# Performance work log

Hardware: AMD Instinct MI355X
Metric: run time of the kernel (lower is better)

Reference implementation:

```python
import jax, jax.numpy as jnp
import numpy as np

K = 20          # neighbors
EPS = 1e-5      # batch-norm eps (torch default)


def setup_inputs() -> dict:
    key = jax.random.key(0)
    k1, k2 = jax.random.split(key, 2)
    B, C, N = 16, 3, 2048
    out_dims, in_dims = 64, 2 * C
    x = jax.random.normal(k1, (B, C, N), dtype=jnp.float32)
    # Conv2d 1x1 weight, kaiming-style init as in init_layer: std = sqrt(2/(1*1*out))
    W = jax.random.normal(k2, (out_dims, in_dims), dtype=jnp.float32) * np.float32(np.sqrt(2.0 / out_dims))
    bn_weight = jnp.ones((out_dims,), dtype=jnp.float32)
    bn_bias = jnp.zeros((out_dims,), dtype=jnp.float32)
    return {"x": x, "W": W, "bn_weight": bn_weight, "bn_bias": bn_bias}


def _get_graph_feature(x, k):
    # x: (B, C, N)
    xx = jnp.sum(x * x, axis=1)                       # (B, N) squared norms
    inner = jnp.einsum('bcn,bcm->bnm', x, x)          # (B, N, N)
    pd = -xx[:, :, None] + 2.0 * inner - xx[:, None, :]  # -||xi - xj||^2
    _, idx = jax.lax.top_k(pd, k)                     # (B, N, k) nearest neighbors
    xt = jnp.transpose(x, (0, 2, 1))                  # (B, N, C)
    # gather neighbor features per batch: (N, C)[ (N, k) ] -> (N, k, C)
    neigh = jax.vmap(lambda feats, ind: feats[ind])(xt, idx)   # (B, N, k, C)
    center = jnp.broadcast_to(xt[:, :, None, :], neigh.shape)  # (B, N, k, C)
    feat = jnp.concatenate([neigh - center, center], axis=-1)  # (B, N, k, 2C)
    return jnp.transpose(feat, (0, 3, 1, 2))          # (B, 2C, N, k)


def reference(x, W, bn_weight, bn_bias):
    feat = _get_graph_feature(x, K)                   # (B, 2C, N, k)
    y = jnp.einsum('oc,bcnk->bonk', W, feat)          # 1x1 conv, no bias
    # BatchNorm2d_fw: fresh running stats + training=True -> plain batch stats
    mean = jnp.mean(y, axis=(0, 2, 3), keepdims=True)
    var = jnp.var(y, axis=(0, 2, 3), keepdims=True)   # biased variance
    yn = (y - mean) * jax.lax.rsqrt(var + EPS)
    yn = yn * bn_weight[None, :, None, None] + bn_bias[None, :, None, None]
    out = jnp.max(jax.nn.relu(yn), axis=-1)           # max over k -> (B, 64, N)
    return out
```

## Files before the change

### kernel.cpp

```cpp
#include <hip/hip_runtime.h>
#include <math.h>

#define B_   16
#define N_   2048
#define KNN  20
#define OD   64
#define M_TOT (B_ * N_ * KNN)
#define PPB  64
#define NB   64
#define CAP  89
#define BKT_BASE 468

typedef unsigned long long u64;
typedef unsigned int u32;

__global__ __launch_bounds__(256, 2) void k1_knn(const float* __restrict__ x,
                                                 float* __restrict__ stats,
                                                 int* __restrict__ idxbuf) {
    __shared__ float4 pts[N_];
    __shared__ u64    coll[PPB][CAP];
    __shared__ u32    pcnt[PPB];
    __shared__ u32    edgev[PPB];

    u32* hist = (u32*)&coll[0][0];

    const int b     = blockIdx.x >> 5;
    const int chunk = blockIdx.x & 31;
    const int t     = threadIdx.x;

    const float* xb = x + b * 3 * N_;
    for (int n = t; n < N_; n += 256) {
        float x0 = xb[n], x1 = xb[N_ + n], x2 = xb[2 * N_ + n];
        float xx = x0 * x0;
        xx = fmaf(x1, x1, xx);
        xx = fmaf(x2, x2, xx);
        pts[n] = make_float4(x0, x1, x2, xx);
    }
    {
        uint4* h4 = (uint4*)hist;
        for (int i = t; i < NB * PPB / 4; i += 256) h4[i] = make_uint4(0, 0, 0, 0);
        if (t < PPB) pcnt[t] = 0;
    }
    __syncthreads();

    const int p  = t & 63;
    const int s  = t >> 6;
    const int il = chunk * 64 + p;
    const float4 pi = pts[il];
    const int j0 = s << 9;

    {
        auto binit = [&](const float4& pj) {
            float dot = pi.x * pj.x;
            dot = fmaf(pi.y, pj.y, dot);
            dot = fmaf(pi.z, pj.z, dot);
            float pd = fmaf(2.f, dot, -pi.w) - pj.w;
            u32 nk = __float_as_uint(pd) & 0x7FFFFFFFu;
            int bkt = (int)(nk >> 21) - BKT_BASE;
            bkt = min(max(bkt, 0), 63);
            atomicAdd(&hist[bkt * PPB + p], 1u);
        };
        for (int jj = 0; jj < 512; jj += 4) {
            int j = j0 + jj;
            float4 q0 = pts[j + 0];
            float4 q1 = pts[j + 1];
            float4 q2 = pts[j + 2];
            float4 q3 = pts[j + 3];
            binit(q0); binit(q1); binit(q2); binit(q3);
        }
    }
    __syncthreads();

    if (t < PPB) {
        int cum = 0, tau = 63;
        for (int k = 0; k < NB; ++k) {
            cum += (int)hist[k * PPB + t];
            if (cum >= KNN) { tau = k; break; }
        }
        edgev[t] = (u32)(BKT_BASE + 1 + tau) << 21;
    }
    __syncthreads();

    {
        const u32 edge = edgev[p];
        auto collect = [&](const float4& pj, int j) {
            float dot = pi.x * pj.x;
            dot = fmaf(pi.y, pj.y, dot);
            dot = fmaf(pi.z, pj.z, dot);
            float pd = fmaf(2.f, dot, -pi.w) - pj.w;
            u32 u = __float_as_uint(pd);
            u32 nk = u & 0x7FFFFFFFu;
            if (nk < edge) {
                u32 mono = ((int)u < 0) ? ~u : (u | 0x80000000u);
                u64 key = ((u64)mono << 32) | (u32)(~j);
                u32 pos = atomicAdd(&pcnt[p], 1u);
                if (pos < CAP) coll[p][pos] = key;
            }
        };
        for (int jj = 0; jj < 512; jj += 4) {
            int j = j0 + jj;
            float4 q0 = pts[j + 0];
            float4 q1 = pts[j + 1];
            float4 q2 = pts[j + 2];
            float4 q3 = pts[j + 3];
            collect(q0, j + 0); collect(q1, j + 1);
            collect(q2, j + 2); collect(q3, j + 3);
        }
    }
    __syncthreads();

    if (t < PPB) {
        const int cnt = min((int)pcnt[t], CAP);
        u64 d[KNN];
#pragma unroll
        for (int q = 0; q < KNN; ++q) d[q] = 0ull;
        for (int e = 0; e < cnt; ++e) {
            u64 v = coll[t][e];
#pragma unroll
            for (int q = 0; q < KNN; ++q) {
                u64 hi = (v > d[q]) ? v : d[q];
                u64 lo = (v > d[q]) ? d[q] : v;
                d[q] = hi; v = lo;
            }
        }
        int ri[KNN];
#pragma unroll
        for (int r = 0; r < KNN; ++r) ri[r] = ~(u32)d[r];

        int* op = idxbuf + (b * N_ + il) * KNN;
#pragma unroll
        for (int r = 0; r < KNN; ++r) op[r] = ri[r];

        float se0 = 0.f, se1 = 0.f, se2 = 0.f;
        float see[6] = {0.f, 0.f, 0.f, 0.f, 0.f, 0.f};
#pragma unroll
        for (int r = 0; r < KNN; ++r) {
            float4 pj = pts[ri[r]];
            float e0 = pj.x - pi.x, e1 = pj.y - pi.y, e2 = pj.z - pi.z;
            se0 += e0; se1 += e1; se2 += e2;
            see[0] = fmaf(e0, e0, see[0]);
            see[1] = fmaf(e0, e1, see[1]);
            see[2] = fmaf(e0, e2, see[2]);
            see[3] = fmaf(e1, e1, see[3]);
            see[4] = fmaf(e1, e2, see[4]);
            see[5] = fmaf(e2, e2, see[5]);
        }
        float c0 = pi.x, c1 = pi.y, c2 = pi.z;
        float v[27];
        v[0] = se0; v[1] = se1; v[2] = se2;
        v[3] = 20.f * c0; v[4] = 20.f * c1; v[5] = 20.f * c2;
        v[6]  = see[0];
        v[7]  = see[1];
        v[8]  = see[2];
        v[9]  = se0 * c0;
        v[10] = se0 * c1;
        v[11] = se0 * c2;
        v[12] = see[3];
        v[13] = see[4];
        v[14] = se1 * c0;
        v[15] = se1 * c1;
        v[16] = se1 * c2;
        v[17] = see[5];
        v[18] = se2 * c0;
        v[19] = se2 * c1;
        v[20] = se2 * c2;
        v[21] = 20.f * c0 * c0;
        v[22] = 20.f * c0 * c1;
        v[23] = 20.f * c0 * c2;
        v[24] = 20.f * c1 * c1;
        v[25] = 20.f * c1 * c2;
        v[26] = 20.f * c2 * c2;

#pragma unroll
        for (int m = 0; m < 27; ++m) {
            float sm = v[m];
#pragma unroll
            for (int off = 32; off > 0; off >>= 1) sm += __shfl_xor(sm, off);
            if (t == 0) atomicAdd(stats + m, sm);
        }
    }
}

__global__ void k2_fin(const float* __restrict__ stats, const float* __restrict__ W,
                       const float* __restrict__ bnw, const float* __restrict__ bnb,
                       float* __restrict__ wp) {
    const int o = threadIdx.x;
    float m[6];
#pragma unroll
    for (int c = 0; c < 6; ++c) m[c] = stats[c];
    float S[6][6];
    int p = 6;
#pragma unroll
    for (int a = 0; a < 6; ++a)
#pragma unroll
        for (int bb = a; bb < 6; ++bb) { S[a][bb] = stats[p]; S[bb][a] = stats[p]; ++p; }
    float w[6];
#pragma unroll
    for (int c = 0; c < 6; ++c) w[c] = W[o * 6 + c];

    const float invM = 1.f / (float)M_TOT;
    float mean = 0.f;
#pragma unroll
    for (int c = 0; c < 6; ++c) mean += w[c] * m[c];
    mean *= invM;
    float ey2 = 0.f;
#pragma unroll
    for (int a = 0; a < 6; ++a)
#pragma unroll
        for (int bb = 0; bb < 6; ++bb) ey2 += w[a] * w[bb] * S[a][bb];
    ey2 *= invM;
    float var   = ey2 - mean * mean;
    float scale = bnw[o] * rsqrtf(var + 1e-5f);
    float shift = bnb[o] - mean * scale;
#pragma unroll
    for (int c = 0; c < 6; ++c) wp[o * 8 + c] = w[c] * scale;
    wp[o * 8 + 6] = shift;
    wp[o * 8 + 7] = 0.f;
}

__global__ __launch_bounds__(256) void k3_out(const float* __restrict__ x,
                                              const float* __restrict__ wp,
                                              const int* __restrict__ idxbuf,
                                              float* __restrict__ out) {
    __shared__ float4 pts[N_];
    __shared__ float  lwp[OD * 8];

    const int b     = blockIdx.x >> 4;
    const int chunk = blockIdx.x & 15;
    const int t     = threadIdx.x;

    const float* xb = x + b * 3 * N_;
    for (int n = t; n < N_; n += 256)
        pts[n] = make_float4(xb[n], xb[N_ + n], xb[2 * N_ + n], 0.f);
    for (int q = t; q < OD * 8; q += 256) lwp[q] = wp[q];
    __syncthreads();

    const int n = chunk * 128 + (t & 127);
    const int h = t >> 7;
    const float4 pi = pts[n];
    const int* ip = idxbuf + (b * N_ + n) * KNN;

    float e0[KNN], e1[KNN], e2[KNN];
#pragma unroll
    for (int r = 0; r < KNN; ++r) {
        int j = ip[r];
        float4 pj = pts[j];
        e0[r] = pj.x - pi.x;
        e1[r] = pj.y - pi.y;
        e2[r] = pj.z - pi.z;
    }

    float* ob = out + (size_t)b * OD * N_ + n;
    const int o0 = h * 32;
#pragma unroll 8
    for (int o = o0; o < o0 + 32; ++o) {
        float w0 = lwp[o * 8 + 0], w1 = lwp[o * 8 + 1], w2 = lwp[o * 8 + 2];
        float w3 = lwp[o * 8 + 3], w4 = lwp[o * 8 + 4], w5 = lwp[o * 8 + 5];
        float base = lwp[o * 8 + 6];
        base = fmaf(w3, pi.x, base);
        base = fmaf(w4, pi.y, base);
        base = fmaf(w5, pi.z, base);
        float acc = 0.f;
#pragma unroll
        for (int r = 0; r < KNN; ++r) {
            float y = base;
            y = fmaf(w0, e0[r], y);
            y = fmaf(w1, e1[r], y);
            y = fmaf(w2, e2[r], y);
            acc = fmaxf(acc, y);
        }
        ob[(size_t)o * N_] = acc;
    }
}

extern "C" void kernel_launch(void* const* d_in, const int* in_sizes, int n_in,
                              void* d_out, int out_size, void* d_ws, size_t ws_size,
                              hipStream_t stream) {
    const float* x   = (const float*)d_in[0];
    const float* W   = (const float*)d_in[1];
    const float* bnw = (const float*)d_in[2];
    const float* bnb = (const float*)d_in[3];
    float* out = (float*)d_out;

    float* stats  = (float*)d_ws;
    float* wp     = (float*)((char*)d_ws + 1024);
    int*   idxbuf = (int*)((char*)d_ws + 4096);

    hipMemsetAsync(d_ws, 0, 128, stream);
    k1_knn<<<dim3(512), dim3(256), 0, stream>>>(x, stats, idxbuf);
    k2_fin<<<dim3(1), dim3(64), 0, stream>>>(stats, W, bnw, bnb, wp);
    k3_out<<<dim3(256), dim3(256), 0, stream>>>(x, wp, idxbuf, out);
}
```

Before: 264.9 us.

## Widen kNN blocks, store 16-bit candidate indices, recompute distances in selection

k1 now runs 512 threads per block, so each point's candidate scan is split across 8 slices of 256 instead of 4 of 512. Candidates are stored as 16-bit indices instead of 64-bit keys, which shrinks shared memory and allows a separate histogram buffer. Distances are recomputed in the single-thread selection phase, and an early reject against the current 20th-best skips the insertion network. k3 uses 512 blocks of 64 points with indices staged in shared memory and 16 outputs per thread. The cost is recomputing distances in the selection phase, which is still serial, and k1 now carries a 4-blocks-per-SM launch bound on 512-thread blocks.

```diff
diff --git a/kernel.cpp b/kernel.cpp
--- a/kernel.cpp
+++ b/kernel.cpp
@@ -8,65 +8,58 @@
 #define M_TOT (B_ * N_ * KNN)
 #define PPB  64
 #define NB   64
-#define CAP  89
+#define CAP  96
 #define BKT_BASE 468
 
 typedef unsigned long long u64;
 typedef unsigned int u32;
-
-__global__ __launch_bounds__(256, 2) void k1_knn(const float* __restrict__ x,
+typedef unsigned short u16;
+
+__global__ __launch_bounds__(512, 4) void k1_knn(const float* __restrict__ x,
                                                  float* __restrict__ stats,
                                                  int* __restrict__ idxbuf) {
     __shared__ float4 pts[N_];
-    __shared__ u64    coll[PPB][CAP];
+    __shared__ u32    hist[NB * PPB];
+    __shared__ u16    coll[PPB][CAP];
     __shared__ u32    pcnt[PPB];
     __shared__ u32    edgev[PPB];
-
-    u32* hist = (u32*)&coll[0][0];
 
     const int b     = blockIdx.x >> 5;
     const int chunk = blockIdx.x & 31;
     const int t     = threadIdx.x;
 
     const float* xb = x + b * 3 * N_;
-    for (int n = t; n < N_; n += 256) {
+    for (int n = t; n < N_; n += 512) {
         float x0 = xb[n], x1 = xb[N_ + n], x2 = xb[2 * N_ + n];
         float xx = x0 * x0;
         xx = fmaf(x1, x1, xx);
         xx = fmaf(x2, x2, xx);
         pts[n] = make_float4(x0, x1, x2, xx);
     }
-    {
-        uint4* h4 = (uint4*)hist;
-        for (int i = t; i < NB * PPB / 4; i += 256) h4[i] = make_uint4(0, 0, 0, 0);
-        if (t < PPB) pcnt[t] = 0;
-    }
+    for (int i = t; i < NB * PPB; i += 512) hist[i] = 0;
+    if (t < PPB) pcnt[t] = 0;
     __syncthreads();
 
     const int p  = t & 63;
     const int s  = t >> 6;
     const int il = chunk * 64 + p;
     const float4 pi = pts[il];
-    const int j0 = s << 9;
-
-    {
-        auto binit = [&](const float4& pj) {
-            float dot = pi.x * pj.x;
-            dot = fmaf(pi.y, pj.y, dot);
-            dot = fmaf(pi.z, pj.z, dot);
-            float pd = fmaf(2.f, dot, -pi.w) - pj.w;
+    const int j0 = s << 8;
+
+    for (int jj = 0; jj < 256; jj += 8) {
+        float4 q[8];
+#pragma unroll
+        for (int u = 0; u < 8; ++u) q[u] = pts[j0 + jj + u];
+#pragma unroll
+        for (int u = 0; u < 8; ++u) {
+            float dot = pi.x * q[u].x;
+            dot = fmaf(pi.y, q[u].y, dot);
+            dot = fmaf(pi.z, q[u].z, dot);
+            float pd = fmaf(2.f, dot, -pi.w) - q[u].w;
             u32 nk = __float_as_uint(pd) & 0x7FFFFFFFu;
             int bkt = (int)(nk >> 21) - BKT_BASE;
             bkt = min(max(bkt, 0), 63);
             atomicAdd(&hist[bkt * PPB + p], 1u);
-        };
-        for (int jj = 0; jj < 512; jj += 4) {
-            int j = j0 + jj;
-            float4 q0 = pts[j + 0];
-            float4 q1 = pts[j + 1];
-            float4 q2 = pts[j + 2];
-            float4 q3 = pts[j + 3];
-            binit(q0); binit(q1); binit(q2); binit(q3);
         }
     }
     __syncthreads();
@@ -83,44 +76,48 @@
 
     {
         const u32 edge = edgev[p];
-        auto collect = [&](const float4& pj, int j) {
+        for (int jj = 0; jj < 256; jj += 8) {
+            float4 q[8];
+#pragma unroll
+            for (int u = 0; u < 8; ++u) q[u] = pts[j0 + jj + u];
+#pragma unroll
+            for (int u = 0; u < 8; ++u) {
+                float dot = pi.x * q[u].x;
+                dot = fmaf(pi.y, q[u].y, dot);
+                dot = fmaf(pi.z, q[u].z, dot);
+                float pd = fmaf(2.f, dot, -pi.w) - q[u].w;
+                u32 nk = __float_as_uint(pd) & 0x7FFFFFFFu;
+                if (nk < edge) {
+                    u32 pos = atomicAdd(&pcnt[p], 1u);
+                    if (pos < CAP) coll[p][pos] = (u16)(j0 + jj + u);
+                }
+            }
+        }
+    }
+    __syncthreads();
+
+    if (t < PPB) {
+        const int cnt = min((int)pcnt[t], CAP);
+        u64 d[KNN];
+#pragma unroll
+        for (int q = 0; q < KNN; ++q) d[q] = 0ull;
+        for (int e = 0; e < cnt; ++e) {
+            int j = coll[t][e];
+            float4 pj = pts[j];
             float dot = pi.x * pj.x;
             dot = fmaf(pi.y, pj.y, dot);
             dot = fmaf(pi.z, pj.z, dot);
             float pd = fmaf(2.f, dot, -pi.w) - pj.w;
             u32 u = __float_as_uint(pd);
-            u32 nk = u & 0x7FFFFFFFu;
-            if (nk < edge) {
-                u32 mono = ((int)u < 0) ? ~u : (u | 0x80000000u);
-                u64 key = ((u64)mono << 32) | (u32)(~j);
-                u32 pos = atomicAdd(&pcnt[p], 1u);
-                if (pos < CAP) coll[p][pos] = key;
-            }
-        };
-        for (int jj = 0; jj < 512; jj += 4) {
-            int j = j0 + jj;
-            float4 q0 = pts[j + 0];
-            float4 q1 = pts[j + 1];
-            float4 q2 = pts[j + 2];
-            float4 q3 = pts[j + 3];
-            collect(q0, j + 0); collect(q1, j + 1);
-            collect(q2, j + 2); collect(q3, j + 3);
-        }
-    }
-    __syncthreads();
-
-    if (t < PPB) {
-        const int cnt = min((int)pcnt[t], CAP);
-        u64 d[KNN];
-#pragma unroll
-        for (int q = 0; q < KNN; ++q) d[q] = 0ull;
-        for (int e = 0; e < cnt; ++e) {
-            u64 v = coll[t][e];
-#pragma unroll
-            for (int q = 0; q < KNN; ++q) {
-                u64 hi = (v > d[q]) ? v : d[q];
-                u64 lo = (v > d[q]) ? d[q] : v;
-                d[q] = hi; v = lo;
+            u32 mono = ((int)u < 0) ? ~u : (u | 0x80000000u);
+            u64 v = ((u64)mono << 32) | (u32)(~j);
+            if (v > d[KNN - 1]) {
+#pragma unroll
+                for (int q = 0; q < KNN; ++q) {
+                    u64 hi = (v > d[q]) ? v : d[q];
+                    u64 lo = (v > d[q]) ? d[q] : v;
+                    d[q] = hi; v = lo;
+                }
             }
         }
         int ri[KNN];
@@ -218,32 +215,37 @@
     wp[o * 8 + 7] = 0.f;
 }
 
-__global__ __launch_bounds__(256) void k3_out(const float* __restrict__ x,
-                                              const float* __restrict__ wp,
-                                              const int* __restrict__ idxbuf,
-                                              float* __restrict__ out) {
+__global__ __launch_bounds__(256, 2) void k3_out(const float* __restrict__ x,
+                                                 const float* __restrict__ wp,
+                                                 const int* __restrict__ idxbuf,
+                                                 float* __restrict__ out) {
     __shared__ float4 pts[N_];
     __shared__ float  lwp[OD * 8];
-
-    const int b     = blockIdx.x >> 4;
-    const int chunk = blockIdx.x & 15;
+    __shared__ int    sidx[PPB * KNN];
+
+    const int b     = blockIdx.x >> 5;
+    const int chunk = blockIdx.x & 31;
     const int t     = threadIdx.x;
 
     const float* xb = x + b * 3 * N_;
     for (int n = t; n < N_; n += 256)
         pts[n] = make_float4(xb[n], xb[N_ + n], xb[2 * N_ + n], 0.f);
     for (int q = t; q < OD * 8; q += 256) lwp[q] = wp[q];
-    __syncthreads();
-
-    const int n = chunk * 128 + (t & 127);
-    const int h = t >> 7;
+    {
+        const int* ib = idxbuf + (b * N_ + chunk * 64) * KNN;
+        for (int i = t; i < PPB * KNN; i += 256) sidx[i] = ib[i];
+    }
+    __syncthreads();
+
+    const int nl  = t & 63;
+    const int sub = t >> 6;
+    const int n   = chunk * 64 + nl;
     const float4 pi = pts[n];
-    const int* ip = idxbuf + (b * N_ + n) * KNN;
 
     float e0[KNN], e1[KNN], e2[KNN];
 #pragma unroll
     for (int r = 0; r < KNN; ++r) {
-        int j = ip[r];
+        int j = sidx[nl * KNN + r];
         float4 pj = pts[j];
         e0[r] = pj.x - pi.x;
         e1[r] = pj.y - pi.y;
@@ -251,9 +253,9 @@
     }
 
     float* ob = out + (size_t)b * OD * N_ + n;
-    const int o0 = h * 32;
-#pragma unroll 8
-    for (int o = o0; o < o0 + 32; ++o) {
+    const int o0 = sub * 16;
+#pragma unroll 4
+    for (int o = o0; o < o0 + 16; ++o) {
         float w0 = lwp[o * 8 + 0], w1 = lwp[o * 8 + 1], w2 = lwp[o * 8 + 2];
         float w3 = lwp[o * 8 + 3], w4 = lwp[o * 8 + 4], w5 = lwp[o * 8 + 5];
         float base = lwp[o * 8 + 6];
@@ -287,7 +289,7 @@
     int*   idxbuf = (int*)((char*)d_ws + 4096);
 
     hipMemsetAsync(d_ws, 0, 128, stream);
-    k1_knn<<<dim3(512), dim3(256), 0, stream>>>(x, stats, idxbuf);
+    k1_knn<<<dim3(512), dim3(512), 0, stream>>>(x, stats, idxbuf);
     k2_fin<<<dim3(1), dim3(64), 0, stream>>>(stats, W, bnw, bnb, wp);
-    k3_out<<<dim3(256), dim3(256), 0, stream>>>(x, wp, idxbuf, out);
-}
+    k3_out<<<dim3(512), dim3(256), 0, stream>>>(x, wp, idxbuf, out);
+}
```

After: 236.0 us. -10.9%, faster.
